# Kernel tuning notes

Measured on AMD Instinct MI355X. Metric: run time of the kernel, lower is better.

## Reference

```python
import jax, jax.numpy as jnp
import numpy as np
from jax import lax

P = 16            # patch_size
EMB = 768         # embedding_dim
CH = 1            # channel
PAD = P // 2 + P // 4  # 12, as in the torch module
FLAT = P * P * CH


def setup_inputs() -> dict:
    key = jax.random.key(0)
    k1, k2, k3, k4, k5 = jax.random.split(key, 5)
    B, T, H, W = 32, 4096, 512, 512
    input_batch = jax.random.normal(k1, (B, CH, H, W), dtype=jnp.float32)
    keypointSequence = jax.random.randint(k2, (B, T, 2), 0, 512, dtype=jnp.int32)
    # torch code does random.randint(0, P//4) per (b,t) -> values 0..4 inclusive
    shifts = jax.random.randint(k3, (B, T, 2), 0, P // 4 + 1, dtype=jnp.int32)
    Wlin = jax.random.normal(k4, (EMB, FLAT), dtype=jnp.float32) * 0.02
    blin = jax.random.normal(k5, (EMB,), dtype=jnp.float32) * 0.02
    return {"input_batch": input_batch, "keypointSequence": keypointSequence,
            "shifts": shifts, "Wlin": Wlin, "blin": blin}


def _slice_patch(padded_img, y0, x0):
    # padded_img: [C, Hp, Wp]; y0, x0 scalar ints -> [C, P, P]
    return lax.dynamic_slice(padded_img, (0, y0, x0), (CH, P, P))


def reference(input_batch, keypointSequence, shifts, Wlin, blin):
    B = input_batch.shape[0]
    T = keypointSequence.shape[1]
    # zero pad H and W by PAD on each side
    padded = jnp.pad(input_batch, ((0, 0), (0, 0), (PAD, PAD), (PAD, PAD)))
    # in the torch code: start = center + shift (the -p//2 + p//2 cancels)
    starts = keypointSequence + shifts            # [B, T, 2] (x, y)
    x0 = starts[..., 0]
    y0 = starts[..., 1]
    # vectorized patch gather: vmap over T, then over B
    patches = jax.vmap(jax.vmap(_slice_patch, in_axes=(None, 0, 0)),
                       in_axes=(0, 0, 0))(padded, y0, x0)  # [B, T, C, P, P]
    flat = patches.reshape(B, T, -1, FLAT)        # [B, T, 1, FLAT]
    # nn.Linear: x @ W.T + b
    return jnp.einsum('btcf,ef->btce', flat, Wlin) + blin
```

## Files before the change

kernel.cpp:

```cpp
#include <hip/hip_runtime.h>
#include <stdint.h>

#define IMG_H   512
#define IMG_W   512
#define PADDING 12
#define EMB     768
#define FLAT    256
#define MTILE   64
#define LDA     264

typedef __attribute__((ext_vector_type(8))) short short8;
typedef __attribute__((ext_vector_type(4))) float floatx4;

__device__ __forceinline__ ushort f2bf(float f) {
  union { float f; uint32_t i; } c; c.f = f;
  uint32_t u = c.i + 0x7FFFu + ((c.i >> 16) & 1u);
  return (ushort)(u >> 16);
}

__global__ __launch_bounds__(256) void convert_w_kernel(
    const float* __restrict__ W, ushort* __restrict__ Wb) {
  int i = (blockIdx.x * 256 + threadIdx.x) * 8;
  float4 a = *(const float4*)(W + i);
  float4 b = *(const float4*)(W + i + 4);
  short8 t;
  t[0] = (short)f2bf(a.x); t[1] = (short)f2bf(a.y);
  t[2] = (short)f2bf(a.z); t[3] = (short)f2bf(a.w);
  t[4] = (short)f2bf(b.x); t[5] = (short)f2bf(b.y);
  t[6] = (short)f2bf(b.z); t[7] = (short)f2bf(b.w);
  *(short8*)(Wb + i) = t;
}

__global__ __launch_bounds__(256) void patch_embed_kernel(
    const float*  __restrict__ img,
    const int*    __restrict__ kp,
    const int*    __restrict__ sh,
    const ushort* __restrict__ Wb,
    const float*  __restrict__ bl,
    float*        __restrict__ out)
{
  __shared__ __align__(16) ushort A[MTILE * LDA];
  __shared__ int sx[MTILE], sy[MTILE];

  const int tid = threadIdx.x;
  const int m0  = blockIdx.x * MTILE;

  if (tid < MTILE) {
    int m = m0 + tid;
    sx[tid] = kp[2 * m]     + sh[2 * m];
    sy[tid] = kp[2 * m + 1] + sh[2 * m + 1];
  }
  __syncthreads();

  #pragma unroll
  for (int it = 0; it < 8; it++) {
    int s  = it * 256 + tid;
    int p  = s >> 5;
    int q  = s & 31;
    int r  = q >> 1;
    int c0 = (q & 1) << 3;
    int y  = sy[p] + r  - PADDING;
    int xb = sx[p] + c0 - PADDING;
    int b  = (m0 + p) >> 12;
    bool rowok = (y >= 0) & (y < IMG_H);
    int  yc = min(max(y, 0), IMG_H - 1);
    size_t base = ((size_t)b * (size_t)(IMG_H * IMG_W)) + (size_t)yc * IMG_W;
    uint32_t pk[4];
    #pragma unroll
    for (int j = 0; j < 4; j++) {
      int x0 = xb + 2 * j, x1 = x0 + 1;
      bool ok0 = rowok & (x0 >= 0) & (x0 < IMG_W);
      bool ok1 = rowok & (x1 >= 0) & (x1 < IMG_W);
      int x0c = min(max(x0, 0), IMG_W - 1);
      int x1c = min(max(x1, 0), IMG_W - 1);
      float f0 = img[base + x0c], f1 = img[base + x1c];
      ushort v0 = ok0 ? f2bf(f0) : (ushort)0;
      ushort v1 = ok1 ? f2bf(f1) : (ushort)0;
      pk[j] = (uint32_t)v0 | ((uint32_t)v1 << 16);
    }
    uint32_t* dst = (uint32_t*)&A[p * LDA + q * 8];
    dst[0] = pk[0]; dst[1] = pk[1]; dst[2] = pk[2]; dst[3] = pk[3];
  }
  __syncthreads();

  const int lane = tid & 63;
  const int w    = tid >> 6;
  const int lm   = lane & 15;
  const int kq   = lane >> 4;

  for (int ec = 0; ec < 3; ec++) {
    const int e0 = ec * 256 + w * 64;
    floatx4 acc[4][4];
    #pragma unroll
    for (int mi = 0; mi < 4; mi++)
      #pragma unroll
      for (int ni = 0; ni < 4; ni++)
        acc[mi][ni] = (floatx4){0.f, 0.f, 0.f, 0.f};

    #pragma unroll
    for (int kk = 0; kk < 8; kk++) {
      short8 af[4], bfr[4];
      #pragma unroll
      for (int mi = 0; mi < 4; mi++)
        af[mi] = *(const short8*)&A[(mi * 16 + lm) * LDA + kk * 32 + kq * 8];
      #pragma unroll
      for (int ni = 0; ni < 4; ni++)
        bfr[ni] = *(const short8*)&Wb[(size_t)(e0 + ni * 16 + lm) * FLAT + kk * 32 + kq * 8];
      #pragma unroll
      for (int mi = 0; mi < 4; mi++)
        #pragma unroll
        for (int ni = 0; ni < 4; ni++)
          acc[mi][ni] = __builtin_amdgcn_mfma_f32_16x16x32_bf16(af[mi], bfr[ni], acc[mi][ni], 0, 0, 0);
    }

    #pragma unroll
    for (int ni = 0; ni < 4; ni++) {
      int e = e0 + ni * 16 + lm;
      float bias = bl[e];
      #pragma unroll
      for (int mi = 0; mi < 4; mi++) {
        int mbase = m0 + mi * 16 + kq * 4;
        #pragma unroll
        for (int rg = 0; rg < 4; rg++)
          out[(size_t)(mbase + rg) * EMB + e] = acc[mi][ni][rg] + bias;
      }
    }
  }
}

extern "C" void kernel_launch(void* const* d_in, const int* in_sizes, int n_in,
                              void* d_out, int out_size, void* d_ws, size_t ws_size,
                              hipStream_t stream) {
  const float* img = (const float*)d_in[0];
  const int*   kp  = (const int*)d_in[1];
  const int*   sh  = (const int*)d_in[2];
  const float* Wl  = (const float*)d_in[3];
  const float* bl  = (const float*)d_in[4];
  float*       out = (float*)d_out;
  ushort*      Wb  = (ushort*)d_ws;

  hipLaunchKernelGGL(convert_w_kernel, dim3(96), dim3(256), 0, stream, Wl, Wb);

  const int Mtotal = 32 * 4096;
  hipLaunchKernelGGL(patch_embed_kernel, dim3(Mtotal / MTILE), dim3(256), 0, stream,
                     img, kp, sh, Wb, bl, out);
}
```

Measured before the change: 585.4 us.

## Split patch gather and GEMM into separate kernels via workspace staging

The fused gather+GEMM kernel is split in two. A standalone gather kernel writes bf16 patch tiles, already padded to the LDS layout, into a workspace buffer. A GEMM kernel then loads each tile into LDS using global_load_lds DMA and runs the MFMA loop. The MFMA loop is also reordered to load one B fragment at a time, which cuts register pressure. The aim is to decouple the latency-bound scattered gather from the compute phase so each runs at full occupancy, at the cost of an extra round trip of about 75MB through global memory. The fused path is kept as a fallback when the workspace is too small.

```diff
diff --git a/kernel.cpp b/kernel.cpp
--- a/kernel.cpp
+++ b/kernel.cpp
@@ -8,6 +8,9 @@
 #define FLAT    256
 #define MTILE   64
 #define LDA     264
+#define NTILES  2048
+#define TILE_WS 36864
+#define WB_BYTES 393216
 
 typedef __attribute__((ext_vector_type(8))) short short8;
 typedef __attribute__((ext_vector_type(4))) float floatx4;
@@ -31,40 +34,137 @@
   *(short8*)(Wb + i) = t;
 }
 
-__global__ __launch_bounds__(256) void patch_embed_kernel(
-    const float*  __restrict__ img,
-    const int*    __restrict__ kp,
-    const int*    __restrict__ sh,
+__global__ __launch_bounds__(256) void gather_kernel(
+    const float* __restrict__ img,
+    const int*   __restrict__ kp,
+    const int*   __restrict__ sh,
+    ushort*      __restrict__ wsA)
+{
+  int gid = blockIdx.x * 256 + threadIdx.x;
+  int m = gid >> 5;
+  int q = gid & 31;
+  int2 k2 = *(const int2*)(kp + 2 * (size_t)m);
+  int2 s2 = *(const int2*)(sh + 2 * (size_t)m);
+  int r  = q >> 1;
+  int c0 = (q & 1) << 3;
+  int y  = k2.y + s2.y + r  - PADDING;
+  int xb = k2.x + s2.x + c0 - PADDING;
+  int b  = m >> 12;
+  bool rowok = (y >= 0) & (y < IMG_H);
+  int  yc = min(max(y, 0), IMG_H - 1);
+  const float* rp = img + (size_t)b * (size_t)(IMG_H * IMG_W) + (size_t)yc * IMG_W;
+  uint32_t pk[4];
+  #pragma unroll
+  for (int j = 0; j < 4; j++) {
+    int x0 = xb + 2 * j, x1 = x0 + 1;
+    bool ok0 = rowok & (x0 >= 0) & (x0 < IMG_W);
+    bool ok1 = rowok & (x1 >= 0) & (x1 < IMG_W);
+    int x0c = min(max(x0, 0), IMG_W - 1);
+    int x1c = min(max(x1, 0), IMG_W - 1);
+    float f0 = rp[x0c], f1 = rp[x1c];
+    ushort v0 = ok0 ? f2bf(f0) : (ushort)0;
+    ushort v1 = ok1 ? f2bf(f1) : (ushort)0;
+    pk[j] = (uint32_t)v0 | ((uint32_t)v1 << 16);
+  }
+  int t = m >> 6, p = m & 63;
+  uint32_t* dst = (uint32_t*)((char*)wsA + (size_t)t * TILE_WS + p * 528 + q * 16);
+  dst[0] = pk[0]; dst[1] = pk[1]; dst[2] = pk[2]; dst[3] = pk[3];
+}
+
+__global__ __launch_bounds__(256) void gemm_kernel(
+    const ushort* __restrict__ wsA,
     const ushort* __restrict__ Wb,
     const float*  __restrict__ bl,
     float*        __restrict__ out)
 {
+  __shared__ __align__(16) ushort A[TILE_WS / 2];
+
+  const int tid  = threadIdx.x;
+  const int lane = tid & 63;
+  const int w    = tid >> 6;
+  const int t    = blockIdx.x;
+  const int m0   = t * MTILE;
+
+  const char* gsrc = (const char*)wsA + (size_t)t * TILE_WS + w * 1024 + lane * 16;
+  char*       ldst = (char*)A + w * 1024;
+  #pragma unroll
+  for (int it = 0; it < 9; it++) {
+    __builtin_amdgcn_global_load_lds(
+        (const __attribute__((address_space(1))) uint32_t*)(gsrc + it * 4096),
+        (__attribute__((address_space(3))) uint32_t*)(ldst + it * 4096),
+        16, 0, 0);
+  }
+  asm volatile("s_waitcnt vmcnt(0)");
+  __syncthreads();
+
+  const int lm = lane & 15;
+  const int kq = lane >> 4;
+
+  for (int ec = 0; ec < 3; ec++) {
+    const int e0 = ec * 256 + w * 64;
+    floatx4 acc[4][4];
+    #pragma unroll
+    for (int mi = 0; mi < 4; mi++)
+      #pragma unroll
+      for (int ni = 0; ni < 4; ni++)
+        acc[mi][ni] = (floatx4){0.f, 0.f, 0.f, 0.f};
+
+    #pragma unroll
+    for (int kk = 0; kk < 8; kk++) {
+      short8 af[4];
+      #pragma unroll
+      for (int mi = 0; mi < 4; mi++)
+        af[mi] = *(const short8*)&A[(mi * 16 + lm) * LDA + kk * 32 + kq * 8];
+      #pragma unroll
+      for (int ni = 0; ni < 4; ni++) {
+        short8 bfr = *(const short8*)&Wb[(size_t)(e0 + ni * 16 + lm) * FLAT + kk * 32 + kq * 8];
+        #pragma unroll
+        for (int mi = 0; mi < 4; mi++)
+          acc[mi][ni] = __builtin_amdgcn_mfma_f32_16x16x32_bf16(af[mi], bfr, acc[mi][ni], 0, 0, 0);
+      }
+    }
+
+    #pragma unroll
+    for (int ni = 0; ni < 4; ni++) {
+      int e = e0 + ni * 16 + lm;
+      float bias = bl[e];
+      #pragma unroll
+      for (int mi = 0; mi < 4; mi++) {
+        int mbase = m0 + mi * 16 + kq * 4;
+        #pragma unroll
+        for (int rg = 0; rg < 4; rg++)
+          out[(size_t)(mbase + rg) * EMB + e] = acc[mi][ni][rg] + bias;
+      }
+    }
+  }
+}
+
+__global__ __launch_bounds__(256) void patch_embed_fused(
+    const float*  __restrict__ img, const int* __restrict__ kp,
+    const int*    __restrict__ sh,  const ushort* __restrict__ Wb,
+    const float*  __restrict__ bl,  float* __restrict__ out)
+{
   __shared__ __align__(16) ushort A[MTILE * LDA];
   __shared__ int sx[MTILE], sy[MTILE];
-
   const int tid = threadIdx.x;
   const int m0  = blockIdx.x * MTILE;
-
   if (tid < MTILE) {
     int m = m0 + tid;
     sx[tid] = kp[2 * m]     + sh[2 * m];
     sy[tid] = kp[2 * m + 1] + sh[2 * m + 1];
   }
   __syncthreads();
-
   #pragma unroll
   for (int it = 0; it < 8; it++) {
     int s  = it * 256 + tid;
-    int p  = s >> 5;
-    int q  = s & 31;
-    int r  = q >> 1;
-    int c0 = (q & 1) << 3;
+    int p  = s >> 5, q = s & 31;
+    int r  = q >> 1, c0 = (q & 1) << 3;
     int y  = sy[p] + r  - PADDING;
     int xb = sx[p] + c0 - PADDING;
     int b  = (m0 + p) >> 12;
     bool rowok = (y >= 0) & (y < IMG_H);
     int  yc = min(max(y, 0), IMG_H - 1);
-    size_t base = ((size_t)b * (size_t)(IMG_H * IMG_W)) + (size_t)yc * IMG_W;
+    const float* rp = img + (size_t)b * (size_t)(IMG_H * IMG_W) + (size_t)yc * IMG_W;
     uint32_t pk[4];
     #pragma unroll
     for (int j = 0; j < 4; j++) {
@@ -73,7 +173,7 @@
       bool ok1 = rowok & (x1 >= 0) & (x1 < IMG_W);
       int x0c = min(max(x0, 0), IMG_W - 1);
       int x1c = min(max(x1, 0), IMG_W - 1);
-      float f0 = img[base + x0c], f1 = img[base + x1c];
+      float f0 = rp[x0c], f1 = rp[x1c];
       ushort v0 = ok0 ? f2bf(f0) : (ushort)0;
       ushort v1 = ok1 ? f2bf(f1) : (ushort)0;
       pk[j] = (uint32_t)v0 | ((uint32_t)v1 << 16);
@@ -82,12 +182,8 @@
     dst[0] = pk[0]; dst[1] = pk[1]; dst[2] = pk[2]; dst[3] = pk[3];
   }
   __syncthreads();
-
-  const int lane = tid & 63;
-  const int w    = tid >> 6;
-  const int lm   = lane & 15;
-  const int kq   = lane >> 4;
-
+  const int lane = tid & 63, w = tid >> 6;
+  const int lm = lane & 15, kq = lane >> 4;
   for (int ec = 0; ec < 3; ec++) {
     const int e0 = ec * 256 + w * 64;
     floatx4 acc[4][4];
@@ -96,23 +192,20 @@
       #pragma unroll
       for (int ni = 0; ni < 4; ni++)
         acc[mi][ni] = (floatx4){0.f, 0.f, 0.f, 0.f};
-
     #pragma unroll
     for (int kk = 0; kk < 8; kk++) {
-      short8 af[4], bfr[4];
+      short8 af[4];
       #pragma unroll
       for (int mi = 0; mi < 4; mi++)
         af[mi] = *(const short8*)&A[(mi * 16 + lm) * LDA + kk * 32 + kq * 8];
       #pragma unroll
-      for (int ni = 0; ni < 4; ni++)
-        bfr[ni] = *(const short8*)&Wb[(size_t)(e0 + ni * 16 + lm) * FLAT + kk * 32 + kq * 8];
-      #pragma unroll
-      for (int mi = 0; mi < 4; mi++)
-        #pragma unroll
-        for (int ni = 0; ni < 4; ni++)
-          acc[mi][ni] = __builtin_amdgcn_mfma_f32_16x16x32_bf16(af[mi], bfr[ni], acc[mi][ni], 0, 0, 0);
-    }
-
+      for (int ni = 0; ni < 4; ni++) {
+        short8 bfr = *(const short8*)&Wb[(size_t)(e0 + ni * 16 + lm) * FLAT + kk * 32 + kq * 8];
+        #pragma unroll
+        for (int mi = 0; mi < 4; mi++)
+          acc[mi][ni] = __builtin_amdgcn_mfma_f32_16x16x32_bf16(af[mi], bfr, acc[mi][ni], 0, 0, 0);
+      }
+    }
     #pragma unroll
     for (int ni = 0; ni < 4; ni++) {
       int e = e0 + ni * 16 + lm;
@@ -138,10 +231,18 @@
   const float* bl  = (const float*)d_in[4];
   float*       out = (float*)d_out;
   ushort*      Wb  = (ushort*)d_ws;
+  ushort*      wsA = (ushort*)((char*)d_ws + WB_BYTES);
 
   hipLaunchKernelGGL(convert_w_kernel, dim3(96), dim3(256), 0, stream, Wl, Wb);
 
-  const int Mtotal = 32 * 4096;
-  hipLaunchKernelGGL(patch_embed_kernel, dim3(Mtotal / MTILE), dim3(256), 0, stream,
-                     img, kp, sh, Wb, bl, out);
-}
+  const size_t need = (size_t)WB_BYTES + (size_t)NTILES * TILE_WS;
+  if (ws_size >= need) {
+    hipLaunchKernelGGL(gather_kernel, dim3(131072 * 32 / 256), dim3(256), 0, stream,
+                       img, kp, sh, wsA);
+    hipLaunchKernelGGL(gemm_kernel, dim3(NTILES), dim3(256), 0, stream,
+                       wsA, Wb, bl, out);
+  } else {
+    hipLaunchKernelGGL(patch_embed_fused, dim3(NTILES), dim3(256), 0, stream,
+                       img, kp, sh, Wb, bl, out);
+  }
+}
```

Result: slower. 674.8 us (+15.3%).

## Split M tile into halves and overlap second-half gather with first GEMM

Applied to the files above, without the earlier changes.

The 64-row patch tile is split into two 32-row halves in separate LDS buffers. Gather loads for the second half are issued into registers before the first half's MFMA GEMM runs, then converted and stored to LDS afterwards, so global-load latency hides behind compute. It also hoists the batch image base pointer out of the loop. In exchange, register pressure rises (32 floats plus masks held across the GEMM), occupancy may drop, and each W fragment is now reused across 2 M-subtiles instead of 4, doubling W reads from L2.

```diff
diff --git a/kernel.cpp b/kernel.cpp
--- a/kernel.cpp
+++ b/kernel.cpp
@@ -7,7 +7,9 @@
 #define EMB     768
 #define FLAT    256
 #define MTILE   64
+#define HALF    32
 #define LDA     264
+#define WB_BYTES 393216
 
 typedef __attribute__((ext_vector_type(8))) short short8;
 typedef __attribute__((ext_vector_type(4))) float floatx4;
@@ -39,11 +41,13 @@
     const float*  __restrict__ bl,
     float*        __restrict__ out)
 {
-  __shared__ __align__(16) ushort A[MTILE * LDA];
+  __shared__ __align__(16) ushort A0[HALF * LDA];
+  __shared__ __align__(16) ushort A1[HALF * LDA];
   __shared__ int sx[MTILE], sy[MTILE];
 
   const int tid = threadIdx.x;
   const int m0  = blockIdx.x * MTILE;
+  const float* ib = img + (size_t)(m0 >> 12) * (size_t)(IMG_H * IMG_W);
 
   if (tid < MTILE) {
     int m = m0 + tid;
@@ -53,7 +57,7 @@
   __syncthreads();
 
   #pragma unroll
-  for (int it = 0; it < 8; it++) {
+  for (int it = 0; it < 4; it++) {
     int s  = it * 256 + tid;
     int p  = s >> 5;
     int q  = s & 31;
@@ -61,10 +65,9 @@
     int c0 = (q & 1) << 3;
     int y  = sy[p] + r  - PADDING;
     int xb = sx[p] + c0 - PADDING;
-    int b  = (m0 + p) >> 12;
     bool rowok = (y >= 0) & (y < IMG_H);
     int  yc = min(max(y, 0), IMG_H - 1);
-    size_t base = ((size_t)b * (size_t)(IMG_H * IMG_W)) + (size_t)yc * IMG_W;
+    const float* rp = ib + (size_t)yc * IMG_W;
     uint32_t pk[4];
     #pragma unroll
     for (int j = 0; j < 4; j++) {
@@ -73,14 +76,45 @@
       bool ok1 = rowok & (x1 >= 0) & (x1 < IMG_W);
       int x0c = min(max(x0, 0), IMG_W - 1);
       int x1c = min(max(x1, 0), IMG_W - 1);
-      float f0 = img[base + x0c], f1 = img[base + x1c];
+      float f0 = rp[x0c], f1 = rp[x1c];
       ushort v0 = ok0 ? f2bf(f0) : (ushort)0;
       ushort v1 = ok1 ? f2bf(f1) : (ushort)0;
       pk[j] = (uint32_t)v0 | ((uint32_t)v1 << 16);
     }
-    uint32_t* dst = (uint32_t*)&A[p * LDA + q * 8];
+    uint32_t* dst = (uint32_t*)&A0[p * LDA + q * 8];
     dst[0] = pk[0]; dst[1] = pk[1]; dst[2] = pk[2]; dst[3] = pk[3];
   }
+
+  float g0[4][4], g1[4][4];
+  uint32_t okm[4];
+  #pragma unroll
+  for (int it = 0; it < 4; it++) {
+    int s  = it * 256 + tid;
+    int p  = 32 + (s >> 5);
+    int q  = s & 31;
+    int r  = q >> 1;
+    int c0 = (q & 1) << 3;
+    int y  = sy[p] + r  - PADDING;
+    int xb = sx[p] + c0 - PADDING;
+    bool rowok = (y >= 0) & (y < IMG_H);
+    int  yc = min(max(y, 0), IMG_H - 1);
+    const float* rp = ib + (size_t)yc * IMG_W;
+    uint32_t mbits = 0;
+    #pragma unroll
+    for (int j = 0; j < 4; j++) {
+      int x0 = xb + 2 * j, x1 = x0 + 1;
+      bool ok0 = rowok & (x0 >= 0) & (x0 < IMG_W);
+      bool ok1 = rowok & (x1 >= 0) & (x1 < IMG_W);
+      int x0c = min(max(x0, 0), IMG_W - 1);
+      int x1c = min(max(x1, 0), IMG_W - 1);
+      g0[it][j] = rp[x0c];
+      g1[it][j] = rp[x1c];
+      mbits |= (ok0 ? 1u : 0u) << (2 * j);
+      mbits |= (ok1 ? 1u : 0u) << (2 * j + 1);
+    }
+    okm[it] = mbits;
+  }
+
   __syncthreads();
 
   const int lane = tid & 63;
@@ -88,44 +122,66 @@
   const int lm   = lane & 15;
   const int kq   = lane >> 4;
 
-  for (int ec = 0; ec < 3; ec++) {
-    const int e0 = ec * 256 + w * 64;
-    floatx4 acc[4][4];
+  auto gemm_half = [&](const ushort* Ab, int mbase) {
+    for (int ec = 0; ec < 3; ec++) {
+      const int e0 = ec * 256 + w * 64;
+      floatx4 acc[2][4];
+      #pragma unroll
+      for (int mi = 0; mi < 2; mi++)
+        #pragma unroll
+        for (int ni = 0; ni < 4; ni++)
+          acc[mi][ni] = (floatx4){0.f, 0.f, 0.f, 0.f};
+
+      #pragma unroll
+      for (int kk = 0; kk < 8; kk++) {
+        short8 af[2];
+        #pragma unroll
+        for (int mi = 0; mi < 2; mi++)
+          af[mi] = *(const short8*)&Ab[(mi * 16 + lm) * LDA + kk * 32 + kq * 8];
+        #pragma unroll
+        for (int ni = 0; ni < 4; ni++) {
+          short8 bfr = *(const short8*)&Wb[(size_t)(e0 + ni * 16 + lm) * FLAT + kk * 32 + kq * 8];
+          #pragma unroll
+          for (int mi = 0; mi < 2; mi++)
+            acc[mi][ni] = __builtin_amdgcn_mfma_f32_16x16x32_bf16(af[mi], bfr, acc[mi][ni], 0, 0, 0);
+        }
+      }
+
+      #pragma unroll
+      for (int ni = 0; ni < 4; ni++) {
+        int e = e0 + ni * 16 + lm;
+        float bias = bl[e];
+        #pragma unroll
+        for (int mi = 0; mi < 2; mi++) {
+          int mb = mbase + mi * 16 + kq * 4;
+          #pragma unroll
+          for (int rg = 0; rg < 4; rg++)
+            out[(size_t)(mb + rg) * EMB + e] = acc[mi][ni][rg] + bias;
+        }
+      }
+    }
+  };
+
+  gemm_half(A0, m0);
+
+  #pragma unroll
+  for (int it = 0; it < 4; it++) {
+    int s = it * 256 + tid;
+    int p = s >> 5;
+    int q = s & 31;
+    uint32_t pk[4];
     #pragma unroll
-    for (int mi = 0; mi < 4; mi++)
-      #pragma unroll
-      for (int ni = 0; ni < 4; ni++)
-        acc[mi][ni] = (floatx4){0.f, 0.f, 0.f, 0.f};
-
-    #pragma unroll
-    for (int kk = 0; kk < 8; kk++) {
-      short8 af[4], bfr[4];
-      #pragma unroll
-      for (int mi = 0; mi < 4; mi++)
-        af[mi] = *(const short8*)&A[(mi * 16 + lm) * LDA + kk * 32 + kq * 8];
-      #pragma unroll
-      for (int ni = 0; ni < 4; ni++)
-        bfr[ni] = *(const short8*)&Wb[(size_t)(e0 + ni * 16 + lm) * FLAT + kk * 32 + kq * 8];
-      #pragma unroll
-      for (int mi = 0; mi < 4; mi++)
-        #pragma unroll
-        for (int ni = 0; ni < 4; ni++)
-          acc[mi][ni] = __builtin_amdgcn_mfma_f32_16x16x32_bf16(af[mi], bfr[ni], acc[mi][ni], 0, 0, 0);
-    }
-
-    #pragma unroll
-    for (int ni = 0; ni < 4; ni++) {
-      int e = e0 + ni * 16 + lm;
-      float bias = bl[e];
-      #pragma unroll
-      for (int mi = 0; mi < 4; mi++) {
-        int mbase = m0 + mi * 16 + kq * 4;
-        #pragma unroll
-        for (int rg = 0; rg < 4; rg++)
-          out[(size_t)(mbase + rg) * EMB + e] = acc[mi][ni][rg] + bias;
-      }
-    }
-  }
+    for (int j = 0; j < 4; j++) {
+      ushort v0 = ((okm[it] >> (2 * j))     & 1u) ? f2bf(g0[it][j]) : (ushort)0;
+      ushort v1 = ((okm[it] >> (2 * j + 1)) & 1u) ? f2bf(g1[it][j]) : (ushort)0;
+      pk[j] = (uint32_t)v0 | ((uint32_t)v1 << 16);
+    }
+    uint32_t* dst = (uint32_t*)&A1[p * LDA + q * 8];
+    dst[0] = pk[0]; dst[1] = pk[1]; dst[2] = pk[2]; dst[3] = pk[3];
+  }
+  __syncthreads();
+
+  gemm_half(A1, m0 + HALF);
 }
 
 extern "C" void kernel_launch(void* const* d_in, const int* in_sizes, int n_in,
```

After: 616.8 us. 5.4% more time.
